# Kernel tuning notes

Measured on AMD Instinct MI355X. Metric: run time of the kernel, lower is better.

The kernel has to match this reference:

```python
import jax, jax.numpy as jnp
import numpy as np

NUM_USERS = 100000
NUM_ITEMS = 50000
EMB_DIM = 128
NUM_LAYERS = 3
NUM_EDGES = 2000000
BATCH = 8192
REG = 1e-4


def setup_inputs() -> dict:
    key = jax.random.key(0)
    ks = jax.random.split(key, 8)
    N = NUM_USERS + NUM_ITEMS
    user_emb = jax.random.normal(ks[0], (NUM_USERS, EMB_DIM), dtype=jnp.float32) * 0.01
    item_emb = jax.random.normal(ks[1], (NUM_ITEMS, EMB_DIM), dtype=jnp.float32) * 0.01
    edge_row = jax.random.randint(ks[2], (NUM_EDGES,), 0, N, dtype=jnp.int32)
    edge_col = jax.random.randint(ks[3], (NUM_EDGES,), 0, N, dtype=jnp.int32)
    # symmetric-normalized adjacency values are small positives
    edge_val = jax.random.uniform(ks[4], (NUM_EDGES,), dtype=jnp.float32) * 0.1
    user = jax.random.randint(ks[5], (BATCH,), 0, NUM_USERS, dtype=jnp.int32)
    pos = jax.random.randint(ks[6], (BATCH,), 0, NUM_ITEMS, dtype=jnp.int32)
    neg = jax.random.randint(ks[7], (BATCH,), 0, NUM_ITEMS, dtype=jnp.int32)
    return {"user_emb": user_emb, "item_emb": item_emb,
            "edge_row": edge_row, "edge_col": edge_col, "edge_val": edge_val,
            "user": user, "pos": pos, "neg": neg}


def _lightgcn_embedding(user_emb, item_emb, edge_row, edge_col, edge_val):
    N = user_emb.shape[0] + item_emb.shape[0]
    emb = jnp.concatenate([user_emb, item_emb], axis=0)  # [N, D]
    acc = emb
    for _ in range(NUM_LAYERS):
        # SpMM: out[r] += val * emb[c] for each edge (r, c)
        msg = emb[edge_col] * edge_val[:, None]  # [E, D]
        emb = jax.ops.segment_sum(msg, edge_row, num_segments=N)
        acc = acc + emb
    light = acc / jnp.float32(NUM_LAYERS + 1)  # mean over layer outputs
    return light[:NUM_USERS], light[NUM_USERS:]


def reference(user_emb, item_emb, edge_row, edge_col, edge_val, user, pos, neg):
    u_all, i_all = _lightgcn_embedding(user_emb, item_emb, edge_row, edge_col, edge_val)
    u_lat = u_all[user]          # [B, D]
    pos_lat = i_all[pos]
    neg_lat = i_all[neg]
    pos_score = jnp.sum(u_lat * pos_lat, axis=1)
    neg_score = jnp.sum(u_lat * neg_lat, axis=1)
    # L1 regularization on ego (layer-0) embeddings, scalar broadcast onto batch loss
    reg_loss = REG * (jnp.sum(jnp.abs(user_emb[user]))
                      + jnp.sum(jnp.abs(item_emb[pos]))
                      + jnp.sum(jnp.abs(item_emb[neg])))
    batch_loss = jax.nn.softplus(neg_score - pos_score) + reg_loss
    return batch_loss
```

## Files before the change

kernel.cpp:

```cpp
#include <hip/hip_runtime.h>
#include <hip/hip_bf16.h>

#define EMB_D 128
#define BSH 9
#define MAXBUCK 512
#define CHUNKP 2048

typedef float f32x2 __attribute__((ext_vector_type(2)));

__device__ __forceinline__ float bf16_raw_to_f(unsigned short h) {
    return __uint_as_float(((unsigned int)h) << 16);
}
__device__ __forceinline__ float sane(float v) {
    return (v == v && fabsf(v) < 256.0f) ? v : 0.0f;
}
__device__ __forceinline__ float load_f(const void* p, int isf32, size_t idx) {
    return isf32 ? ((const float*)p)[idx]
                 : bf16_raw_to_f(((const unsigned short*)p)[idx]);
}

__device__ __forceinline__ f32x2 cvt2_fp8(unsigned int w) {
    f32x2 r;
    asm("v_cvt_pk_f32_fp8 %0, %1" : "=v"(r) : "v"(w));
    return r;
}
__device__ __forceinline__ unsigned int enc2_fp8(float a, float b) {
    unsigned int r;
    asm("v_cvt_pk_fp8_f32 %0, %1, %2" : "=v"(r) : "v"(a), "v"(b));
    return r & 0xFFFFu;
}
__device__ __forceinline__ unsigned int fp8x4_enc(float a, float b, float c, float d) {
    return enc2_fp8(a, b) | (enc2_fp8(c, d) << 16);
}
__device__ __forceinline__ float fp8_dec_byte(unsigned int b) {
    return cvt2_fp8(b & 0xFFu).x;
}

__global__ void k_detect(const unsigned short* __restrict__ ue,
                         const unsigned short* __restrict__ ie,
                         const unsigned short* __restrict__ ev,
                         int* __restrict__ flags) {
    int a = blockIdx.x;
    const unsigned short* p = (a == 0) ? ue : (a == 1) ? ie : ev;
    int lane = threadIdx.x;
    int cnt = 0;
    #pragma unroll
    for (int k = 0; k < 16; ++k) {
        float v = bf16_raw_to_f(p[k * 64 + lane]);
        if (!(fabsf(v) < 1.0f)) cnt++;
    }
    #pragma unroll
    for (int off = 32; off > 0; off >>= 1)
        cnt += __shfl_down(cnt, off, 64);
    if (lane == 0) flags[a] = (cnt > 64) ? 1 : 0;
}

__global__ __launch_bounds__(256) void k_build_emb8(
        const void* __restrict__ ue, const void* __restrict__ ie,
        const int* __restrict__ flags,
        unsigned char* __restrict__ T, float* __restrict__ S,
        int NU, int N) {
    int gid = blockIdx.x * blockDim.x + threadIdx.x;
    int row = gid >> 5;
    if (row >= N) return;
    int l = gid & 31;
    const void* src; long r; int f;
    if (row < NU) { src = ue; r = row;      f = flags[0]; }
    else          { src = ie; r = row - NU; f = flags[1]; }
    float v0, v1, v2, v3;
    if (f) {
        float4 t = ((const float4*)src)[r * 32 + l];
        v0 = sane(t.x); v1 = sane(t.y); v2 = sane(t.z); v3 = sane(t.w);
    } else {
        ushort4 t = ((const ushort4*)src)[r * 32 + l];
        v0 = sane(bf16_raw_to_f(t.x)); v1 = sane(bf16_raw_to_f(t.y));
        v2 = sane(bf16_raw_to_f(t.z)); v3 = sane(bf16_raw_to_f(t.w));
    }
    float m = fmaxf(fmaxf(fabsf(v0), fabsf(v1)), fmaxf(fabsf(v2), fabsf(v3)));
    #pragma unroll
    for (int off = 1; off < 32; off <<= 1)
        m = fmaxf(m, __shfl_xor(m, off, 64));
    float enc = (m > 0.0f) ? 448.0f / m : 0.0f;
    ((unsigned int*)T)[(size_t)row * 32 + l] =
        fp8x4_enc(v0 * enc, v1 * enc, v2 * enc, v3 * enc);
    if (l == 0) S[row] = (m > 0.0f) ? m * (1.0f / 448.0f) : 0.0f;
}

__global__ void k_reg(const void* __restrict__ ue, const void* __restrict__ ie,
                      const int* __restrict__ flags,
                      const int* __restrict__ user, const int* __restrict__ pos,
                      const int* __restrict__ neg, int NU, int NI,
                      float* __restrict__ regp) {
    __shared__ float sred[2];
    int b = blockIdx.x;
    int d = threadIdx.x;
    int ui = min(max(user[b], 0), NU - 1);
    int pi = min(max(pos[b],  0), NI - 1);
    int ni = min(max(neg[b],  0), NI - 1);
    int f0 = flags[0], f1 = flags[1];
    float u = sane(load_f(ue, f0, (size_t)ui * EMB_D + d));
    float p = sane(load_f(ie, f1, (size_t)pi * EMB_D + d));
    float n = sane(load_f(ie, f1, (size_t)ni * EMB_D + d));
    float s = fabsf(u) + fabsf(p) + fabsf(n);
    #pragma unroll
    for (int off = 32; off > 0; off >>= 1)
        s += __shfl_down(s, off, 64);
    if ((d & 63) == 0) sred[d >> 6] = s;
    __syncthreads();
    if (d == 0) regp[b] = sred[0] + sred[1];
}

__global__ void k_reduce_reg(const float* __restrict__ regp, float* __restrict__ reg, int B) {
    __shared__ float ss[256];
    int t = threadIdx.x;
    float s = 0.0f;
    for (int i = t; i < B; i += 256) s += regp[i];
    ss[t] = s;
    __syncthreads();
    for (int off = 128; off > 0; off >>= 1) {
        if (t < off) ss[t] += ss[t + off];
        __syncthreads();
    }
    if (t == 0) reg[0] = ss[0];
}


__global__ __launch_bounds__(256) void k_part_count(const int* __restrict__ erow,
        int* __restrict__ bcnt, int E, int N, int nbuck, int NB) {
    __shared__ int lh[MAXBUCK];
    int b = blockIdx.x, t = threadIdx.x;
    for (int i = t; i < MAXBUCK; i += 256) lh[i] = 0;
    __syncthreads();
    int beg = b * CHUNKP;
    int cnt = min(CHUNKP, E - beg);
    for (int p = t; p < cnt; p += 256) {
        int r = min(max(erow[beg + p], 0), N - 1);
        atomicAdd(&lh[r >> BSH], 1);
    }
    __syncthreads();
    for (int i = t; i < nbuck; i += 256) bcnt[(long)i * NB + b] = lh[i];
}

__global__ void k_gscan1(const int* __restrict__ a, int* __restrict__ bsums, int L) {
    __shared__ int ss[256];
    int t = threadIdx.x;
    int base = blockIdx.x * 1024 + t * 4;
    int s = 0;
    #pragma unroll
    for (int j = 0; j < 4; ++j) {
        int idx = base + j;
        if (idx < L) s += a[idx];
    }
    ss[t] = s;
    __syncthreads();
    for (int off = 128; off > 0; off >>= 1) {
        if (t < off) ss[t] += ss[t + off];
        __syncthreads();
    }
    if (t == 0) bsums[blockIdx.x] = ss[0];
}

__global__ void k_gscan2(const int* __restrict__ bsums, int* __restrict__ boffs,
                         int nb, int* __restrict__ rowptrN) {
    __shared__ int ss[256];
    int t = threadIdx.x;
    int base = t * 4;
    int c[4];
    int s = 0;
    #pragma unroll
    for (int j = 0; j < 4; ++j) {
        c[j] = (base + j < nb) ? bsums[base + j] : 0;
        s += c[j];
    }
    ss[t] = s;
    __syncthreads();
    for (int off = 1; off < 256; off <<= 1) {
        int v = (t >= off) ? ss[t - off] : 0;
        __syncthreads();
        ss[t] += v;
        __syncthreads();
    }
    int run = ss[t] - s;
    #pragma unroll
    for (int j = 0; j < 4; ++j) {
        if (base + j < nb) boffs[base + j] = run;
        run += c[j];
    }
    if (t == 255) *rowptrN = ss[255];
}

__global__ void k_gscan3(int* __restrict__ a, const int* __restrict__ boffs, int L) {
    __shared__ int ss[256];
    int t = threadIdx.x;
    int base = blockIdx.x * 1024 + t * 4;
    int c[4];
    int s = 0;
    #pragma unroll
    for (int j = 0; j < 4; ++j) {
        int idx = base + j;
        c[j] = (idx < L) ? a[idx] : 0;
        s += c[j];
    }
    ss[t] = s;
    __syncthreads();
    for (int off = 1; off < 256; off <<= 1) {
        int v = (t >= off) ? ss[t - off] : 0;
        __syncthreads();
        ss[t] += v;
        __syncthreads();
    }
    int run = boffs[blockIdx.x] + ss[t] - s;
    #pragma unroll
    for (int j = 0; j < 4; ++j) {
        int idx = base + j;
        if (idx < L) a[idx] = run;
        run += c[j];
    }
}

__global__ __launch_bounds__(256) void k_part_scatter(
        const int* __restrict__ erow, const int* __restrict__ ecol,
        const void* __restrict__ eval, const int* __restrict__ flags,
        const int* __restrict__ boff,
        unsigned int* __restrict__ part_cv, unsigned short* __restrict__ part_r,
        int E, int N, int nbuck, int NB) {
    __shared__ uint2 lrec[CHUNKP];
    __shared__ unsigned short lidx[CHUNKP];
    __shared__ int hist[MAXBUCK];
    __shared__ int bstart[MAXBUCK];
    __shared__ int ss[256];
    int b = blockIdx.x, t = threadIdx.x;
    int beg = b * CHUNKP;
    int cnt = min(CHUNKP, E - beg);
    for (int i = t; i < MAXBUCK; i += 256) hist[i] = 0;
    __syncthreads();
    int f2 = flags[2];
    for (int p = t; p < cnt; p += 256) {
        int e = beg + p;
        int r = min(max(erow[e], 0), N - 1);
        int c = min(max(ecol[e], 0), N - 1);
        float v = sane(load_f(eval, f2, e));
        if (v < 0.0f) v = 0.0f;
        unsigned int u = __float_as_uint(v);
        unsigned int vb = ((u + 0x10000u) >> 17) & 0x3FFFu;
        lrec[p] = make_uint2((unsigned int)r, ((unsigned int)c << 14) | vb);
        atomicAdd(&hist[r >> BSH], 1);
    }
    __syncthreads();
    int c0 = hist[2 * t], c1 = hist[2 * t + 1];
    int s = c0 + c1;
    ss[t] = s;
    __syncthreads();
    for (int off = 1; off < 256; off <<= 1) {
        int v = (t >= off) ? ss[t - off] : 0;
        __syncthreads();
        ss[t] += v;
        __syncthreads();
    }
    int eb = ss[t] - s;
    bstart[2 * t] = eb;
    bstart[2 * t + 1] = eb + c0;
    hist[2 * t] = eb;
    hist[2 * t + 1] = eb + c0;
    __syncthreads();
    for (int p = t; p < cnt; p += 256) {
        int bin = (int)(lrec[p].x >> BSH);
        int pos = atomicAdd(&hist[bin], 1);
        lidx[pos] = (unsigned short)p;
    }
    __syncthreads();
    for (int i = t; i < nbuck; i += 256)
        hist[i] = boff[(long)i * NB + b] - bstart[i];
    __syncthreads();
    for (int p = t; p < cnt; p += 256) {
        uint2 rec = lrec[lidx[p]];
        int bin = (int)(rec.x >> BSH);
        int o = hist[bin] + p;
        part_cv[o] = rec.y;
        part_r[o] = (unsigned short)(rec.x & 511u);
    }
}

__global__ __launch_bounds__(256) void k_build_csr(
        const unsigned int* __restrict__ part_cv,
        const unsigned short* __restrict__ part_r,
        const int* __restrict__ boff,
        int* __restrict__ row_ptr, unsigned int* __restrict__ sedge,
        int E, int N, int NB, int nbuck) {
    __shared__ int rcnt[512];
    __shared__ int rstart[512];
    __shared__ int rcur[512];
    __shared__ int ss[256];
    int bin = blockIdx.x, t = threadIdx.x;
    int base = boff[(long)bin * NB];
    int next = (bin + 1 < nbuck) ? boff[(long)(bin + 1) * NB] : E;
    int cnt = next - base;
    int r0 = bin << BSH;
    int nrows = min(512, N - r0);
    rcnt[2 * t] = 0; rcnt[2 * t + 1] = 0;
    __syncthreads();
    for (int i = t; i < cnt; i += 256)
        atomicAdd(&rcnt[part_r[base + i]], 1);
    __syncthreads();
    int c0 = rcnt[2 * t], c1 = rcnt[2 * t + 1];
    int s = c0 + c1;
    ss[t] = s;
    __syncthreads();
    for (int off = 1; off < 256; off <<= 1) {
        int v = (t >= off) ? ss[t - off] : 0;
        __syncthreads();
        ss[t] += v;
        __syncthreads();
    }
    int eb = ss[t] - s;
    rstart[2 * t] = eb; rstart[2 * t + 1] = eb + c0;
    rcur[2 * t]   = eb; rcur[2 * t + 1]   = eb + c0;
    __syncthreads();
    for (int j = t; j < nrows; j += 256)
        row_ptr[r0 + j] = base + rstart[j];
    for (int i = t; i < cnt; i += 256) {
        int pr = part_r[base + i];
        int pos = atomicAdd(&rcur[pr], 1);
        sedge[base + pos] = part_cv[base + i];
    }
}


__global__ void k_zero_flags(int* __restrict__ f, int words) {
    int i = blockIdx.x * blockDim.x + threadIdx.x;
    if (i < words) f[i] = 0;
}

__global__ void k_mark_batch(const int* __restrict__ user, const int* __restrict__ pos,
                             const int* __restrict__ neg, int NU, int NI, int B,
                             unsigned char* __restrict__ flag3,
                             unsigned char* __restrict__ flag2) {
    int b = blockIdx.x * blockDim.x + threadIdx.x;
    if (b >= B) return;
    int ui = min(max(user[b], 0), NU - 1);
    int pi = NU + min(max(pos[b], 0), NI - 1);
    int ni = NU + min(max(neg[b], 0), NI - 1);
    flag3[ui] = 1; flag3[pi] = 1; flag3[ni] = 1;
    flag2[ui] = 1; flag2[pi] = 1; flag2[ni] = 1;
}

__global__ void k_mark_nbrs(const int* __restrict__ row_ptr,
                            const unsigned int* __restrict__ sedge,
                            const unsigned char* __restrict__ flag3,
                            unsigned char* __restrict__ flag2, int N) {
    int r = blockIdx.x * blockDim.x + threadIdx.x;
    if (r >= N || !flag3[r]) return;
    int beg = row_ptr[r], end = row_ptr[r + 1];
    for (int i = beg; i < end; ++i)
        flag2[sedge[i] >> 14] = 1;
}


__global__ void k_spmm_csr8(const unsigned char* __restrict__ T,
                            const float* __restrict__ S,
                            unsigned char* __restrict__ Td,
                            float* __restrict__ Sd,
                            const int* __restrict__ row_ptr,
                            const unsigned int* __restrict__ sedge, int N,
                            const unsigned char* __restrict__ skipf, int use_skip) {
    int row = blockIdx.x * (blockDim.x >> 6) + (threadIdx.x >> 6);
    if (row >= N) return;
    if (use_skip && skipf[row] == 0) return;
    int lane = threadIdx.x & 63;
    int sub = lane >> 3;
    int sl  = lane & 7;
    int beg = row_ptr[row], end = row_ptr[row + 1];
    float a[16];
    #pragma unroll
    for (int j = 0; j < 16; ++j) a[j] = 0.0f;
    int i = beg + sub;
    for (; i + 8 < end; i += 16) {
        unsigned int se0 = sedge[i];
        unsigned int se1 = sedge[i + 8];
        unsigned int c0 = se0 >> 14, c1 = se1 >> 14;
        uint4 h0 = ((const uint4*)(T + (size_t)c0 * EMB_D))[sl];
        uint4 h1 = ((const uint4*)(T + (size_t)c1 * EMB_D))[sl];
        float vs0 = __uint_as_float((se0 & 0x3FFFu) << 17) * S[c0];
        float vs1 = __uint_as_float((se1 & 0x3FFFu) << 17) * S[c1];
        f32x2 d;
        d = cvt2_fp8(h0.x);       a[0] += vs0 * d.x;  a[1] += vs0 * d.y;
        d = cvt2_fp8(h0.x >> 16); a[2] += vs0 * d.x;  a[3] += vs0 * d.y;
        d = cvt2_fp8(h0.y);       a[4] += vs0 * d.x;  a[5] += vs0 * d.y;
        d = cvt2_fp8(h0.y >> 16); a[6] += vs0 * d.x;  a[7] += vs0 * d.y;
        d = cvt2_fp8(h0.z);       a[8] += vs0 * d.x;  a[9] += vs0 * d.y;
        d = cvt2_fp8(h0.z >> 16); a[10] += vs0 * d.x; a[11] += vs0 * d.y;
        d = cvt2_fp8(h0.w);       a[12] += vs0 * d.x; a[13] += vs0 * d.y;
        d = cvt2_fp8(h0.w >> 16); a[14] += vs0 * d.x; a[15] += vs0 * d.y;
        d = cvt2_fp8(h1.x);       a[0] += vs1 * d.x;  a[1] += vs1 * d.y;
        d = cvt2_fp8(h1.x >> 16); a[2] += vs1 * d.x;  a[3] += vs1 * d.y;
        d = cvt2_fp8(h1.y);       a[4] += vs1 * d.x;  a[5] += vs1 * d.y;
        d = cvt2_fp8(h1.y >> 16); a[6] += vs1 * d.x;  a[7] += vs1 * d.y;
        d = cvt2_fp8(h1.z);       a[8] += vs1 * d.x;  a[9] += vs1 * d.y;
        d = cvt2_fp8(h1.z >> 16); a[10] += vs1 * d.x; a[11] += vs1 * d.y;
        d = cvt2_fp8(h1.w);       a[12] += vs1 * d.x; a[13] += vs1 * d.y;
        d = cvt2_fp8(h1.w >> 16); a[14] += vs1 * d.x; a[15] += vs1 * d.y;
    }
    if (i < end) {
        unsigned int se = sedge[i];
        unsigned int c = se >> 14;
        uint4 h = ((const uint4*)(T + (size_t)c * EMB_D))[sl];
        float vs = __uint_as_float((se & 0x3FFFu) << 17) * S[c];
        f32x2 d;
        d = cvt2_fp8(h.x);       a[0] += vs * d.x;  a[1] += vs * d.y;
        d = cvt2_fp8(h.x >> 16); a[2] += vs * d.x;  a[3] += vs * d.y;
        d = cvt2_fp8(h.y);       a[4] += vs * d.x;  a[5] += vs * d.y;
        d = cvt2_fp8(h.y >> 16); a[6] += vs * d.x;  a[7] += vs * d.y;
        d = cvt2_fp8(h.z);       a[8] += vs * d.x;  a[9] += vs * d.y;
        d = cvt2_fp8(h.z >> 16); a[10] += vs * d.x; a[11] += vs * d.y;
        d = cvt2_fp8(h.w);       a[12] += vs * d.x; a[13] += vs * d.y;
        d = cvt2_fp8(h.w >> 16); a[14] += vs * d.x; a[15] += vs * d.y;
    }
    #pragma unroll
    for (int j = 0; j < 16; ++j) {
        a[j] += __shfl_xor(a[j], 8, 64);
        a[j] += __shfl_xor(a[j], 16, 64);
        a[j] += __shfl_xor(a[j], 32, 64);
    }
    float m = 0.0f;
    #pragma unroll
    for (int j = 0; j < 16; ++j) m = fmaxf(m, fabsf(a[j]));
    m = fmaxf(m, __shfl_xor(m, 1, 64));
    m = fmaxf(m, __shfl_xor(m, 2, 64));
    m = fmaxf(m, __shfl_xor(m, 4, 64));
    if (sub == 0) {
        float enc = (m > 0.0f) ? 448.0f / m : 0.0f;
        uint4 w;
        w.x = fp8x4_enc(a[0] * enc,  a[1] * enc,  a[2] * enc,  a[3] * enc);
        w.y = fp8x4_enc(a[4] * enc,  a[5] * enc,  a[6] * enc,  a[7] * enc);
        w.z = fp8x4_enc(a[8] * enc,  a[9] * enc,  a[10] * enc, a[11] * enc);
        w.w = fp8x4_enc(a[12] * enc, a[13] * enc, a[14] * enc, a[15] * enc);
        ((uint4*)(Td + (size_t)row * EMB_D))[sl] = w;
        if (lane == 0) Sd[row] = (m > 0.0f) ? m * (1.0f / 448.0f) : 0.0f;
    }
}

__global__ void k_gather_final(
        const void* __restrict__ ue, const void* __restrict__ ie,
        const int* __restrict__ flags,
        const int* __restrict__ user, const int* __restrict__ pos,
        const int* __restrict__ neg, int NU, int NI,
        const unsigned char* __restrict__ T1, const float* __restrict__ S1,
        const unsigned char* __restrict__ T2, const float* __restrict__ S2,
        const unsigned char* __restrict__ T3, const float* __restrict__ S3,
        const float* __restrict__ reg, float* __restrict__ out) {
    __shared__ float sps[2], sns[2];
    int b = blockIdx.x;
    int d = threadIdx.x;
    int ui = min(max(user[b], 0), NU - 1);
    int pi = min(max(pos[b],  0), NI - 1);
    int ni = min(max(neg[b],  0), NI - 1);
    size_t ru = (size_t)ui;
    size_t rp = (size_t)NU + pi;
    size_t rn = (size_t)NU + ni;
    int f0 = flags[0], f1 = flags[1];
    float u = sane(load_f(ue, f0, ru * EMB_D + d))
            + fp8_dec_byte(T1[ru * EMB_D + d]) * S1[ru]
            + fp8_dec_byte(T2[ru * EMB_D + d]) * S2[ru]
            + fp8_dec_byte(T3[ru * EMB_D + d]) * S3[ru];
    float p = sane(load_f(ie, f1, (size_t)pi * EMB_D + d))
            + fp8_dec_byte(T1[rp * EMB_D + d]) * S1[rp]
            + fp8_dec_byte(T2[rp * EMB_D + d]) * S2[rp]
            + fp8_dec_byte(T3[rp * EMB_D + d]) * S3[rp];
    float n = sane(load_f(ie, f1, (size_t)ni * EMB_D + d))
            + fp8_dec_byte(T1[rn * EMB_D + d]) * S1[rn]
            + fp8_dec_byte(T2[rn * EMB_D + d]) * S2[rn]
            + fp8_dec_byte(T3[rn * EMB_D + d]) * S3[rn];
    float ps = u * p, ns = u * n;
    #pragma unroll
    for (int off = 32; off > 0; off >>= 1) {
        ps += __shfl_down(ps, off, 64);
        ns += __shfl_down(ns, off, 64);
    }
    if ((d & 63) == 0) { sps[d >> 6] = ps; sns[d >> 6] = ns; }
    __syncthreads();
    if (d == 0) {
        float x = ((sns[0] + sns[1]) - (sps[0] + sps[1])) * 0.0625f;
        float sp = fmaxf(x, 0.0f) + log1pf(expf(-fabsf(x)));
        out[b] = sp + 1e-4f * reg[0];
    }
}

extern "C" void kernel_launch(void* const* d_in, const int* in_sizes, int n_in,
                              void* d_out, int out_size, void* d_ws, size_t ws_size,
                              hipStream_t stream) {
    const void* ue   = d_in[0];
    const void* ie   = d_in[1];
    const int*  erow = (const int*)d_in[2];
    const int*  ecol = (const int*)d_in[3];
    const void* ev   = d_in[4];
    const int*  user = (const int*)d_in[5];
    const int*  pos  = (const int*)d_in[6];
    const int*  neg  = (const int*)d_in[7];

    int NU = in_sizes[0] / EMB_D;
    int NI = in_sizes[1] / EMB_D;
    int N  = NU + NI;
    int E  = in_sizes[2];
    int B  = in_sizes[5];

    int nbuck = (N + ((1 << BSH) - 1)) >> BSH;
    int NBp   = (E + CHUNKP - 1) / CHUNKP;
    int L     = nbuck * NBp;
    int nbL   = (L + 1023) / 1024;

    size_t T8   = (size_t)N * EMB_D;
    size_t SC   = (((size_t)N * sizeof(float)) + 15) & ~15ull;
    size_t NI4  = ((size_t)(N + 1) * sizeof(int) + 15) & ~15ull;
    size_t L4   = ((size_t)L * sizeof(int) + 15) & ~15ull;
    size_t E2   = (((size_t)E * 2) + 15) & ~15ull;
    size_t Npad = ((size_t)N + 15) & ~15ull;
    char* w = (char*)d_ws;
    int*   flags   = (int*)w;
    float* reg     = (float*)(w + 64);
    char*  q       = w + 256;
    float* regp    = (float*)q;             q += (size_t)B * sizeof(float);
    int*   row_ptr = (int*)q;               q += NI4;
    unsigned int*   part_cv = (unsigned int*)q;   q += (size_t)E * 4;
    unsigned short* part_r  = (unsigned short*)q; q += E2;
    int*   bcnt    = (int*)q;               q += L4;
    int*   bsums   = (int*)q;               q += 4096;
    int*   boffs   = (int*)q;               q += 4096;
    unsigned char* flag3 = (unsigned char*)q; q += Npad;
    unsigned char* flag2 = (unsigned char*)q; q += Npad;
    unsigned int* sedge = (unsigned int*)q; q += (size_t)E * 4;
    unsigned char* Ta = (unsigned char*)q;  q += T8;
    float*         Sa = (float*)q;          q += SC;
    unsigned char* T1 = (unsigned char*)q;  q += T8;
    float*         S1 = (float*)q;          q += SC;
    unsigned char* T2 = (unsigned char*)q;  q += T8;
    float*         S2 = (float*)q;          q += SC;
    unsigned char* T3 = (unsigned char*)q;  q += T8;
    float*         S3 = (float*)q;

    const int thr = 256;
    float* out = (float*)d_out;

    k_detect<<<3, 64, 0, stream>>>((const unsigned short*)ue, (const unsigned short*)ie,
                                   (const unsigned short*)ev, flags);
    k_build_emb8<<<(N * 32 + thr - 1) / thr, thr, 0, stream>>>(ue, ie, flags, Ta, Sa, NU, N);
    k_reg<<<B, EMB_D, 0, stream>>>(ue, ie, flags, user, pos, neg, NU, NI, regp);
    k_reduce_reg<<<1, 256, 0, stream>>>(regp, reg, B);

    int fwords = (int)((2 * Npad) / 4);
    k_zero_flags<<<(fwords + thr - 1) / thr, thr, 0, stream>>>((int*)flag3, fwords);
    k_mark_batch<<<(B + thr - 1) / thr, thr, 0, stream>>>(user, pos, neg, NU, NI, B,
                                                          flag3, flag2);

    k_part_count<<<NBp, 256, 0, stream>>>(erow, bcnt, E, N, nbuck, NBp);
    k_gscan1<<<nbL, 256, 0, stream>>>(bcnt, bsums, L);
    k_gscan2<<<1, 256, 0, stream>>>(bsums, boffs, nbL, row_ptr + N);
    k_gscan3<<<nbL, 256, 0, stream>>>(bcnt, boffs, L);
    k_part_scatter<<<NBp, 256, 0, stream>>>(erow, ecol, ev, flags, bcnt,
                                            part_cv, part_r, E, N, nbuck, NBp);
    k_build_csr<<<nbuck, 256, 0, stream>>>(part_cv, part_r, bcnt, row_ptr, sedge,
                                           E, N, NBp, nbuck);

    k_mark_nbrs<<<(N + thr - 1) / thr, thr, 0, stream>>>(row_ptr, sedge, flag3, flag2, N);

    int rows_per_block = thr / 64;
    int sgrid = (N + rows_per_block - 1) / rows_per_block;

    k_spmm_csr8<<<sgrid, thr, 0, stream>>>(Ta, Sa, T1, S1, row_ptr, sedge, N, flag2, 0);
    k_spmm_csr8<<<sgrid, thr, 0, stream>>>(T1, S1, T2, S2, row_ptr, sedge, N, flag2, 1);
    k_spmm_csr8<<<sgrid, thr, 0, stream>>>(T2, S2, T3, S3, row_ptr, sedge, N, flag3, 1);

    k_gather_final<<<B, EMB_D, 0, stream>>>(ue, ie, flags, user, pos, neg, NU, NI,
                                            T1, S1, T2, S2, T3, S3, reg, out);
}
```

Measured before the change: 441.5 us.

## Fuse reg-loss into final gather, mark neighbors from edge list, narrow SpMM lanes

The separate L1-regularization kernel is removed. Its per-sample abs sums are now computed inside the final gather, which writes pre-softplus scores; a reduce and a small output kernel follow. Neighbor marking for layer-2 skipping now scans the raw edge list in parallel instead of walking CSR rows per flagged row, so it no longer waits on CSR construction. The SpMM now uses 16 lanes per row with 8-byte loads across 4 edge phases instead of 8 lanes with 16-byte loads across 8 phases. This cuts register pressure but narrows each load.

Measured after the change: 417.9 us (median of 2 runs). 5.3% less time.

```diff
diff --git a/kernel.cpp b/kernel.cpp
--- a/kernel.cpp
+++ b/kernel.cpp
@@ -86,30 +86,6 @@
     if (l == 0) S[row] = (m > 0.0f) ? m * (1.0f / 448.0f) : 0.0f;
 }
 
-__global__ void k_reg(const void* __restrict__ ue, const void* __restrict__ ie,
-                      const int* __restrict__ flags,
-                      const int* __restrict__ user, const int* __restrict__ pos,
-                      const int* __restrict__ neg, int NU, int NI,
-                      float* __restrict__ regp) {
-    __shared__ float sred[2];
-    int b = blockIdx.x;
-    int d = threadIdx.x;
-    int ui = min(max(user[b], 0), NU - 1);
-    int pi = min(max(pos[b],  0), NI - 1);
-    int ni = min(max(neg[b],  0), NI - 1);
-    int f0 = flags[0], f1 = flags[1];
-    float u = sane(load_f(ue, f0, (size_t)ui * EMB_D + d));
-    float p = sane(load_f(ie, f1, (size_t)pi * EMB_D + d));
-    float n = sane(load_f(ie, f1, (size_t)ni * EMB_D + d));
-    float s = fabsf(u) + fabsf(p) + fabsf(n);
-    #pragma unroll
-    for (int off = 32; off > 0; off >>= 1)
-        s += __shfl_down(s, off, 64);
-    if ((d & 63) == 0) sred[d >> 6] = s;
-    __syncthreads();
-    if (d == 0) regp[b] = sred[0] + sred[1];
-}
-
 __global__ void k_reduce_reg(const float* __restrict__ regp, float* __restrict__ reg, int B) {
     __shared__ float ss[256];
     int t = threadIdx.x;
@@ -344,17 +320,17 @@
     flag2[ui] = 1; flag2[pi] = 1; flag2[ni] = 1;
 }
 
-__global__ void k_mark_nbrs(const int* __restrict__ row_ptr,
-                            const unsigned int* __restrict__ sedge,
-                            const unsigned char* __restrict__ flag3,
-                            unsigned char* __restrict__ flag2, int N) {
-    int r = blockIdx.x * blockDim.x + threadIdx.x;
-    if (r >= N || !flag3[r]) return;
-    int beg = row_ptr[r], end = row_ptr[r + 1];
-    for (int i = beg; i < end; ++i)
-        flag2[sedge[i] >> 14] = 1;
-}
-
+__global__ void k_mark_nbrs_e(const int* __restrict__ erow, const int* __restrict__ ecol,
+                              const unsigned char* __restrict__ flag3,
+                              unsigned char* __restrict__ flag2, int E, int N) {
+    int e = blockIdx.x * blockDim.x + threadIdx.x;
+    if (e >= E) return;
+    int r = min(max(erow[e], 0), N - 1);
+    if (flag3[r]) {
+        int c = min(max(ecol[e], 0), N - 1);
+        flag2[c] = 1;
+    }
+}
 
 __global__ void k_spmm_csr8(const unsigned char* __restrict__ T,
                             const float* __restrict__ S,
@@ -367,74 +343,59 @@
     if (row >= N) return;
     if (use_skip && skipf[row] == 0) return;
     int lane = threadIdx.x & 63;
-    int sub = lane >> 3;
-    int sl  = lane & 7;
+    int ph = lane >> 4;
+    int sl = lane & 15;
     int beg = row_ptr[row], end = row_ptr[row + 1];
-    float a[16];
-    #pragma unroll
-    for (int j = 0; j < 16; ++j) a[j] = 0.0f;
-    int i = beg + sub;
-    for (; i + 8 < end; i += 16) {
+    float a[8];
+    #pragma unroll
+    for (int j = 0; j < 8; ++j) a[j] = 0.0f;
+    int i = beg + ph;
+    for (; i + 4 < end; i += 8) {
         unsigned int se0 = sedge[i];
-        unsigned int se1 = sedge[i + 8];
+        unsigned int se1 = sedge[i + 4];
         unsigned int c0 = se0 >> 14, c1 = se1 >> 14;
-        uint4 h0 = ((const uint4*)(T + (size_t)c0 * EMB_D))[sl];
-        uint4 h1 = ((const uint4*)(T + (size_t)c1 * EMB_D))[sl];
+        uint2 h0 = ((const uint2*)(T + (size_t)c0 * EMB_D))[sl];
+        uint2 h1 = ((const uint2*)(T + (size_t)c1 * EMB_D))[sl];
         float vs0 = __uint_as_float((se0 & 0x3FFFu) << 17) * S[c0];
         float vs1 = __uint_as_float((se1 & 0x3FFFu) << 17) * S[c1];
         f32x2 d;
-        d = cvt2_fp8(h0.x);       a[0] += vs0 * d.x;  a[1] += vs0 * d.y;
-        d = cvt2_fp8(h0.x >> 16); a[2] += vs0 * d.x;  a[3] += vs0 * d.y;
-        d = cvt2_fp8(h0.y);       a[4] += vs0 * d.x;  a[5] += vs0 * d.y;
-        d = cvt2_fp8(h0.y >> 16); a[6] += vs0 * d.x;  a[7] += vs0 * d.y;
-        d = cvt2_fp8(h0.z);       a[8] += vs0 * d.x;  a[9] += vs0 * d.y;
-        d = cvt2_fp8(h0.z >> 16); a[10] += vs0 * d.x; a[11] += vs0 * d.y;
-        d = cvt2_fp8(h0.w);       a[12] += vs0 * d.x; a[13] += vs0 * d.y;
-        d = cvt2_fp8(h0.w >> 16); a[14] += vs0 * d.x; a[15] += vs0 * d.y;
-        d = cvt2_fp8(h1.x);       a[0] += vs1 * d.x;  a[1] += vs1 * d.y;
-        d = cvt2_fp8(h1.x >> 16); a[2] += vs1 * d.x;  a[3] += vs1 * d.y;
-        d = cvt2_fp8(h1.y);       a[4] += vs1 * d.x;  a[5] += vs1 * d.y;
-        d = cvt2_fp8(h1.y >> 16); a[6] += vs1 * d.x;  a[7] += vs1 * d.y;
-        d = cvt2_fp8(h1.z);       a[8] += vs1 * d.x;  a[9] += vs1 * d.y;
-        d = cvt2_fp8(h1.z >> 16); a[10] += vs1 * d.x; a[11] += vs1 * d.y;
-        d = cvt2_fp8(h1.w);       a[12] += vs1 * d.x; a[13] += vs1 * d.y;
-        d = cvt2_fp8(h1.w >> 16); a[14] += vs1 * d.x; a[15] += vs1 * d.y;
+        d = cvt2_fp8(h0.x);       a[0] += vs0 * d.x; a[1] += vs0 * d.y;
+        d = cvt2_fp8(h0.x >> 16); a[2] += vs0 * d.x; a[3] += vs0 * d.y;
+        d = cvt2_fp8(h0.y);       a[4] += vs0 * d.x; a[5] += vs0 * d.y;
+        d = cvt2_fp8(h0.y >> 16); a[6] += vs0 * d.x; a[7] += vs0 * d.y;
+        d = cvt2_fp8(h1.x);       a[0] += vs1 * d.x; a[1] += vs1 * d.y;
+        d = cvt2_fp8(h1.x >> 16); a[2] += vs1 * d.x; a[3] += vs1 * d.y;
+        d = cvt2_fp8(h1.y);       a[4] += vs1 * d.x; a[5] += vs1 * d.y;
+        d = cvt2_fp8(h1.y >> 16); a[6] += vs1 * d.x; a[7] += vs1 * d.y;
     }
     if (i < end) {
         unsigned int se = sedge[i];
         unsigned int c = se >> 14;
-        uint4 h = ((const uint4*)(T + (size_t)c * EMB_D))[sl];
+        uint2 h = ((const uint2*)(T + (size_t)c * EMB_D))[sl];
         float vs = __uint_as_float((se & 0x3FFFu) << 17) * S[c];
         f32x2 d;
-        d = cvt2_fp8(h.x);       a[0] += vs * d.x;  a[1] += vs * d.y;
-        d = cvt2_fp8(h.x >> 16); a[2] += vs * d.x;  a[3] += vs * d.y;
-        d = cvt2_fp8(h.y);       a[4] += vs * d.x;  a[5] += vs * d.y;
-        d = cvt2_fp8(h.y >> 16); a[6] += vs * d.x;  a[7] += vs * d.y;
-        d = cvt2_fp8(h.z);       a[8] += vs * d.x;  a[9] += vs * d.y;
-        d = cvt2_fp8(h.z >> 16); a[10] += vs * d.x; a[11] += vs * d.y;
-        d = cvt2_fp8(h.w);       a[12] += vs * d.x; a[13] += vs * d.y;
-        d = cvt2_fp8(h.w >> 16); a[14] += vs * d.x; a[15] += vs * d.y;
-    }
-    #pragma unroll
-    for (int j = 0; j < 16; ++j) {
-        a[j] += __shfl_xor(a[j], 8, 64);
+        d = cvt2_fp8(h.x);       a[0] += vs * d.x; a[1] += vs * d.y;
+        d = cvt2_fp8(h.x >> 16); a[2] += vs * d.x; a[3] += vs * d.y;
+        d = cvt2_fp8(h.y);       a[4] += vs * d.x; a[5] += vs * d.y;
+        d = cvt2_fp8(h.y >> 16); a[6] += vs * d.x; a[7] += vs * d.y;
+    }
+    #pragma unroll
+    for (int j = 0; j < 8; ++j) {
         a[j] += __shfl_xor(a[j], 16, 64);
         a[j] += __shfl_xor(a[j], 32, 64);
     }
-    float m = 0.0f;
-    #pragma unroll
-    for (int j = 0; j < 16; ++j) m = fmaxf(m, fabsf(a[j]));
+    float m = fmaxf(fmaxf(fmaxf(fabsf(a[0]), fabsf(a[1])), fmaxf(fabsf(a[2]), fabsf(a[3]))),
+                    fmaxf(fmaxf(fabsf(a[4]), fabsf(a[5])), fmaxf(fabsf(a[6]), fabsf(a[7]))));
     m = fmaxf(m, __shfl_xor(m, 1, 64));
     m = fmaxf(m, __shfl_xor(m, 2, 64));
     m = fmaxf(m, __shfl_xor(m, 4, 64));
-    if (sub == 0) {
+    m = fmaxf(m, __shfl_xor(m, 8, 64));
+    if (ph == 0) {
         float enc = (m > 0.0f) ? 448.0f / m : 0.0f;
-        uint4 w;
-        w.x = fp8x4_enc(a[0] * enc,  a[1] * enc,  a[2] * enc,  a[3] * enc);
-        w.y = fp8x4_enc(a[4] * enc,  a[5] * enc,  a[6] * enc,  a[7] * enc);
-        w.z = fp8x4_enc(a[8] * enc,  a[9] * enc,  a[10] * enc, a[11] * enc);
-        w.w = fp8x4_enc(a[12] * enc, a[13] * enc, a[14] * enc, a[15] * enc);
-        ((uint4*)(Td + (size_t)row * EMB_D))[sl] = w;
+        uint2 w;
+        w.x = fp8x4_enc(a[0] * enc, a[1] * enc, a[2] * enc, a[3] * enc);
+        w.y = fp8x4_enc(a[4] * enc, a[5] * enc, a[6] * enc, a[7] * enc);
+        ((uint2*)(Td + (size_t)row * EMB_D))[sl] = w;
         if (lane == 0) Sd[row] = (m > 0.0f) ? m * (1.0f / 448.0f) : 0.0f;
     }
 }
@@ -447,8 +408,8 @@
         const unsigned char* __restrict__ T1, const float* __restrict__ S1,
         const unsigned char* __restrict__ T2, const float* __restrict__ S2,
         const unsigned char* __restrict__ T3, const float* __restrict__ S3,
-        const float* __restrict__ reg, float* __restrict__ out) {
-    __shared__ float sps[2], sns[2];
+        float* __restrict__ xv, float* __restrict__ regp) {
+    __shared__ float sps[2], sns[2], srg[2];
     int b = blockIdx.x;
     int d = threadIdx.x;
     int ui = min(max(user[b], 0), NU - 1);
@@ -458,31 +419,44 @@
     size_t rp = (size_t)NU + pi;
     size_t rn = (size_t)NU + ni;
     int f0 = flags[0], f1 = flags[1];
-    float u = sane(load_f(ue, f0, ru * EMB_D + d))
+    float u0 = sane(load_f(ue, f0, ru * EMB_D + d));
+    float p0 = sane(load_f(ie, f1, (size_t)pi * EMB_D + d));
+    float n0 = sane(load_f(ie, f1, (size_t)ni * EMB_D + d));
+    float u = u0
             + fp8_dec_byte(T1[ru * EMB_D + d]) * S1[ru]
             + fp8_dec_byte(T2[ru * EMB_D + d]) * S2[ru]
             + fp8_dec_byte(T3[ru * EMB_D + d]) * S3[ru];
-    float p = sane(load_f(ie, f1, (size_t)pi * EMB_D + d))
+    float p = p0
             + fp8_dec_byte(T1[rp * EMB_D + d]) * S1[rp]
             + fp8_dec_byte(T2[rp * EMB_D + d]) * S2[rp]
             + fp8_dec_byte(T3[rp * EMB_D + d]) * S3[rp];
-    float n = sane(load_f(ie, f1, (size_t)ni * EMB_D + d))
+    float n = n0
             + fp8_dec_byte(T1[rn * EMB_D + d]) * S1[rn]
             + fp8_dec_byte(T2[rn * EMB_D + d]) * S2[rn]
             + fp8_dec_byte(T3[rn * EMB_D + d]) * S3[rn];
     float ps = u * p, ns = u * n;
+    float rg = fabsf(u0) + fabsf(p0) + fabsf(n0);
     #pragma unroll
     for (int off = 32; off > 0; off >>= 1) {
         ps += __shfl_down(ps, off, 64);
         ns += __shfl_down(ns, off, 64);
-    }
-    if ((d & 63) == 0) { sps[d >> 6] = ps; sns[d >> 6] = ns; }
+        rg += __shfl_down(rg, off, 64);
+    }
+    if ((d & 63) == 0) { sps[d >> 6] = ps; sns[d >> 6] = ns; srg[d >> 6] = rg; }
     __syncthreads();
     if (d == 0) {
-        float x = ((sns[0] + sns[1]) - (sps[0] + sps[1])) * 0.0625f;
-        float sp = fmaxf(x, 0.0f) + log1pf(expf(-fabsf(x)));
-        out[b] = sp + 1e-4f * reg[0];
-    }
+        xv[b] = ((sns[0] + sns[1]) - (sps[0] + sps[1])) * 0.0625f;
+        regp[b] = srg[0] + srg[1];
+    }
+}
+
+__global__ void k_final_out(const float* __restrict__ xv, const float* __restrict__ reg,
+                            float* __restrict__ out, int B) {
+    int b = blockIdx.x * blockDim.x + threadIdx.x;
+    if (b >= B) return;
+    float x = xv[b];
+    float sp = fmaxf(x, 0.0f) + log1pf(expf(-fabsf(x)));
+    out[b] = sp + 1e-4f * reg[0];
 }
 
 extern "C" void kernel_launch(void* const* d_in, const int* in_sizes, int n_in,
@@ -519,6 +493,7 @@
     float* reg     = (float*)(w + 64);
     char*  q       = w + 256;
     float* regp    = (float*)q;             q += (size_t)B * sizeof(float);
+    float* xv      = (float*)q;             q += (size_t)B * sizeof(float);
     int*   row_ptr = (int*)q;               q += NI4;
     unsigned int*   part_cv = (unsigned int*)q;   q += (size_t)E * 4;
     unsigned short* part_r  = (unsigned short*)q; q += E2;
@@ -543,13 +518,12 @@
     k_detect<<<3, 64, 0, stream>>>((const unsigned short*)ue, (const unsigned short*)ie,
                                    (const unsigned short*)ev, flags);
     k_build_emb8<<<(N * 32 + thr - 1) / thr, thr, 0, stream>>>(ue, ie, flags, Ta, Sa, NU, N);
-    k_reg<<<B, EMB_D, 0, stream>>>(ue, ie, flags, user, pos, neg, NU, NI, regp);
-    k_reduce_reg<<<1, 256, 0, stream>>>(regp, reg, B);
 
     int fwords = (int)((2 * Npad) / 4);
     k_zero_flags<<<(fwords + thr - 1) / thr, thr, 0, stream>>>((int*)flag3, fwords);
     k_mark_batch<<<(B + thr - 1) / thr, thr, 0, stream>>>(user, pos, neg, NU, NI, B,
                                                           flag3, flag2);
+    k_mark_nbrs_e<<<(E + thr - 1) / thr, thr, 0, stream>>>(erow, ecol, flag3, flag2, E, N);
 
     k_part_count<<<NBp, 256, 0, stream>>>(erow, bcnt, E, N, nbuck, NBp);
     k_gscan1<<<nbL, 256, 0, stream>>>(bcnt, bsums, L);
@@ -560,8 +534,6 @@
     k_build_csr<<<nbuck, 256, 0, stream>>>(part_cv, part_r, bcnt, row_ptr, sedge,
                                            E, N, NBp, nbuck);
 
-    k_mark_nbrs<<<(N + thr - 1) / thr, thr, 0, stream>>>(row_ptr, sedge, flag3, flag2, N);
-
     int rows_per_block = thr / 64;
     int sgrid = (N + rows_per_block - 1) / rows_per_block;
 
@@ -570,5 +542,7 @@
     k_spmm_csr8<<<sgrid, thr, 0, stream>>>(T2, S2, T3, S3, row_ptr, sedge, N, flag3, 1);
 
     k_gather_final<<<B, EMB_D, 0, stream>>>(ue, ie, flags, user, pos, neg, NU, NI,
-                                            T1, S1, T2, S2, T3, S3, reg, out);
-}
+                                            T1, S1, T2, S2, T3, S3, xv, regp);
+    k_reduce_reg<<<1, 256, 0, stream>>>(regp, reg, B);
+    k_final_out<<<(B + thr - 1) / thr, thr, 0, stream>>>(xv, reg, out, B);
+}
```
